# Optimization experiments

Hardware: AMD Instinct MI355X
Metric: run time of the kernel (lower is better)

The kernel has to match this reference:

```python
import jax, jax.numpy as jnp
import numpy as np

DIM = 768
B, S = 16, 1024
EPS = 1e-5


def setup_inputs() -> dict:
    key = jax.random.key(0)
    ks = jax.random.split(key, 13)
    std = 1.0 / np.sqrt(DIM)
    inp = {
        "x_A": jax.random.normal(ks[0], (B, S, DIM), jnp.float32),
        "x_B": jax.random.normal(ks[1], (B, S, DIM), jnp.float32),
        "x_C": jax.random.normal(ks[2], (B, S, DIM), jnp.float32),
        "W_q": jax.random.normal(ks[3], (DIM, DIM), jnp.float32) * std,
        "b_q": jax.random.normal(ks[4], (DIM,), jnp.float32) * std,
        "W_k": jax.random.normal(ks[5], (DIM, DIM), jnp.float32) * std,
        "b_k": jax.random.normal(ks[6], (DIM,), jnp.float32) * std,
        "W_v": jax.random.normal(ks[7], (DIM, DIM), jnp.float32) * std,
        "b_v": jax.random.normal(ks[8], (DIM,), jnp.float32) * std,
        "gamma": jnp.ones((DIM,), jnp.float32),
        "beta": jnp.zeros((DIM,), jnp.float32),
        "W_fc": jax.random.normal(ks[9], (DIM, DIM), jnp.float32) * std,
        "b_fc": jax.random.normal(ks[10], (DIM,), jnp.float32) * std,
    }
    return inp


def _linear(x, W, b):
    # torch nn.Linear: x @ W.T + b
    return jnp.einsum('bsd,ed->bse', x, W) + b


def _layernorm(x, gamma, beta):
    mu = jnp.mean(x, axis=-1, keepdims=True)
    var = jnp.mean((x - mu) ** 2, axis=-1, keepdims=True)
    return (x - mu) * jax.lax.rsqrt(var + EPS) * gamma + beta


def reference(x_A, x_B, x_C, W_q, b_q, W_k, b_k, W_v, b_v, gamma, beta, W_fc, b_fc):
    scale = 1.0 / jnp.sqrt(jnp.float32(DIM))
    Q = _linear(x_C, W_q, b_q)
    K_A = _linear(x_A, W_k, b_k)
    K_B = _linear(x_B, W_k, b_k)
    V_A = _linear(x_A, W_v, b_v)
    V_B = _linear(x_B, W_v, b_v)
    attn_A = jax.nn.softmax(jnp.einsum('bqd,bkd->bqk', Q, K_A) * scale, axis=-1)
    attn_B = jax.nn.softmax(jnp.einsum('bqd,bkd->bqk', Q, K_B) * scale, axis=-1)
    interp_A = jnp.einsum('bqk,bkd->bqd', attn_A, V_A)
    interp_B = jnp.einsum('bqk,bkd->bqd', attn_B, V_B)
    h = _layernorm(interp_A + interp_B + x_C, gamma, beta)
    return _linear(h, W_fc, b_fc)
```

## Files before the change

### kernel.cpp

```cpp
#include <hip/hip_runtime.h>

#define DIMV 768
#define BATCH 16
#define SEQ 1024
#define LN_EPS 1e-5f

typedef __attribute__((ext_vector_type(8))) short bf16x8;
typedef __attribute__((ext_vector_type(4))) float f32x4;
typedef unsigned short ushort_t;

__device__ __forceinline__ unsigned short f2bf(float f) {
    unsigned u = __float_as_uint(f);
    u = (u + 0x7FFFu + ((u >> 16) & 1u)) >> 16;
    return (unsigned short)u;
}


__global__ __launch_bounds__(512, 2) void gemm_bf16_nt_256(
    const ushort_t* __restrict__ A, const ushort_t* __restrict__ B,
    const float* __restrict__ bias, const float* __restrict__ bias2,
    void* __restrict__ Cout, void* __restrict__ Cout2,
    int K, int lda, int ldb, int ldc, float scale, int mode,
    long long sAz, long long sBz, long long sCz, int CbArg)
{
    int bx = blockIdx.x, by = blockIdx.y, bz = blockIdx.z;
    {
        const unsigned Z  = gridDim.z;
        const unsigned nx = gridDim.x, ny = gridDim.y;
        if (Z > 1) {
            const unsigned nxy = nx * ny;
            const unsigned lid = ((unsigned)bz * ny + (unsigned)by) * nx + (unsigned)bx;
            unsigned r;
            if ((Z & 7u) == 0u) {
                const unsigned c  = lid & 7u;
                const unsigned rp = lid >> 3;
                bz = (int)(c + 8u * (rp / nxy));
                r  = rp % nxy;
            } else {
                bz = (int)(lid % Z);
                r  = lid / Z;
            }
            bx = (int)(r % nx);
            by = (int)(r / nx);
        } else {
            const unsigned nwg = nx * ny;
            if ((nwg & 7u) == 0u) {
                const unsigned lid = (unsigned)by * nx + (unsigned)bx;
                const unsigned nl  = (lid & 7u) * (nwg >> 3) + (lid >> 3);
                bx = (int)(nl % nx);
                by = (int)(nl / nx);
            }
        }
    }

    A += (long long)bz * sAz;
    B += (long long)bz * sBz;
    float*    Cf  = (float*)Cout    + ((mode == 0) ? (long long)bz * sCz : 0);
    ushort_t* Ch  = (ushort_t*)Cout + ((mode == 1) ? (long long)bz * sCz : 0);
    ushort_t* Ch2 = (ushort_t*)Cout2;

    __shared__ ushort_t As[4][256 * 32];
    __shared__ ushort_t Bs[4][256 * 32];

    const int t    = threadIdx.x;
    const int wave = t >> 6;
    const int lane = t & 63;
    const int quad = lane >> 4;
    const int lr   = lane & 15;
    const int wy   = wave >> 2;
    const int wx   = wave & 3;

    const int m0 = by * 256;
    const int n0 = bx * 256;

    const ushort_t* Abase = A + (long long)m0 * lda;
    const ushort_t* Bbase = B + (long long)n0 * ldb;

    auto issue = [&](int k0, int slot) {
        #pragma unroll
        for (int i = 0; i < 2; ++i) {
            const int idx = t + 512 * i;
            const int r   = idx >> 2;
            const int q   = idx & 3;
            const int c   = (q ^ ((r >> 1) & 3)) * 8;
            __builtin_amdgcn_global_load_lds(
                (const __attribute__((address_space(1))) unsigned int*)(Abase + (long long)r * lda + k0 + c),
                (__attribute__((address_space(3))) unsigned int*)&As[slot][idx * 8], 16, 0, 0);
            __builtin_amdgcn_global_load_lds(
                (const __attribute__((address_space(1))) unsigned int*)(Bbase + (long long)r * ldb + k0 + c),
                (__attribute__((address_space(3))) unsigned int*)&Bs[slot][idx * 8], 16, 0, 0);
        }
    };

    int offA[8], offB[4];
    #pragma unroll
    for (int i = 0; i < 8; ++i) {
        const int rowA = wy * 128 + i * 16 + lr;
        offA[i] = rowA * 32 + ((quad ^ ((rowA >> 1) & 3)) * 8);
    }
    #pragma unroll
    for (int j = 0; j < 4; ++j) {
        const int rowB = wx * 64 + j * 16 + lr;
        offB[j] = rowB * 32 + ((quad ^ ((rowB >> 1) & 3)) * 8);
    }

    f32x4 acc[8][4] = {};

    const int NK = K >> 5;
    issue(0, 0);
    issue(32, 1);
    for (int ki = 0; ki < NK; ++ki) {
        const int k2 = (ki + 2 < NK) ? (ki + 2) << 5 : (NK - 1) << 5;
        issue(k2, (ki + 2) & 3);
        asm volatile("s_waitcnt vmcnt(8)" ::: "memory");
        asm volatile("s_barrier" ::: "memory");

        const ushort_t* as = &As[ki & 3][0];
        const ushort_t* bs = &Bs[ki & 3][0];
        bf16x8 af[8], bfr[4];
        #pragma unroll
        for (int i = 0; i < 8; ++i) af[i]  = *(const bf16x8*)&as[offA[i]];
        #pragma unroll
        for (int j = 0; j < 4; ++j) bfr[j] = *(const bf16x8*)&bs[offB[j]];

        __builtin_amdgcn_s_setprio(1);
        #pragma unroll
        for (int i = 0; i < 8; ++i)
            #pragma unroll
            for (int j = 0; j < 4; ++j)
                acc[i][j] = __builtin_amdgcn_mfma_f32_16x16x32_bf16(
                    af[i], bfr[j], acc[i][j], 0, 0, 0);
        __builtin_amdgcn_s_setprio(0);
    }

    #pragma unroll
    for (int j = 0; j < 4; ++j) {
        const int n = n0 + wx * 64 + j * 16 + lr;
        float bv;
        if (mode == 4) bv = (n < DIMV) ? bias[n] : bias2[n - DIMV];
        else           bv = bias ? bias[n] : 0.0f;
        #pragma unroll
        for (int i = 0; i < 8; ++i) {
            #pragma unroll
            for (int r = 0; r < 4; ++r) {
                const int m = m0 + wy * 128 + i * 16 + quad * 4 + r;
                const float val = acc[i][j][r] * scale + bv;
                if (mode == 0) {
                    Cf[(long long)m * ldc + n] = val;
                } else if (mode == 1) {
                    Ch[(long long)m * ldc + n] = f2bf(val);
                } else {
                    const int bh = m >> 10, s = m & 1023;
                    const int hf = (bh >= CbArg) ? 1 : 0;
                    const int b  = bh - (hf ? CbArg : 0);
                    if (n < DIMV) {
                        Ch[(long long)b * (2 * SEQ * DIMV) + (long long)(hf * SEQ + s) * DIMV + n] = f2bf(val);
                    } else {
                        Ch2[(long long)b * (2 * SEQ * DIMV) + (long long)(n - DIMV) * (2 * SEQ) + hf * SEQ + s] = f2bf(val);
                    }
                }
            }
        }
    }
}

__global__ __launch_bounds__(256) void gemm_bf16_nt(
    const ushort_t* __restrict__ A, const ushort_t* __restrict__ B,
    const float* __restrict__ bias, void* __restrict__ Cout,
    int K, int lda, int ldb, int ldc, float scale,
    long long sAz, long long sBz, long long sCz)
{
    int bx = blockIdx.x, by = blockIdx.y, bz = blockIdx.z;
    {
        const unsigned Z  = gridDim.z;
        const unsigned nx = gridDim.x, ny = gridDim.y;
        if (Z > 1) {
            const unsigned nxy = nx * ny;
            const unsigned lid = ((unsigned)bz * ny + (unsigned)by) * nx + (unsigned)bx;
            unsigned r;
            if ((Z & 7u) == 0u) {
                const unsigned c  = lid & 7u;
                const unsigned rp = lid >> 3;
                bz = (int)(c + 8u * (rp / nxy));
                r  = rp % nxy;
            } else {
                bz = (int)(lid % Z);
                r  = lid / Z;
            }
            bx = (int)(r % nx);
            by = (int)(r / nx);
        } else {
            const unsigned nwg = nx * ny;
            if ((nwg & 7u) == 0u) {
                const unsigned lid = (unsigned)by * nx + (unsigned)bx;
                const unsigned nl  = (lid & 7u) * (nwg >> 3) + (lid >> 3);
                bx = (int)(nl % nx);
                by = (int)(nl / nx);
            }
        }
    }

    A += (long long)bz * sAz;
    B += (long long)bz * sBz;
    float* Cf = (float*)Cout + (long long)bz * sCz;

    __shared__ ushort_t As[3][128 * 32];
    __shared__ ushort_t Bs[3][128 * 32];

    const int t    = threadIdx.x;
    const int wave = t >> 6;
    const int lane = t & 63;
    const int quad = lane >> 4;
    const int lr   = lane & 15;
    const int wy   = wave >> 1;
    const int wx   = wave & 1;

    const int m0 = by * 128;
    const int n0 = bx * 128;

    const ushort_t* Abase = A + (long long)m0 * lda;
    const ushort_t* Bbase = B + (long long)n0 * ldb;

    auto issue = [&](int k0, int slot) {
        #pragma unroll
        for (int i = 0; i < 2; ++i) {
            const int idx = t + 256 * i;
            const int r   = idx >> 2;
            const int q   = idx & 3;
            const int c   = (q ^ ((r >> 1) & 3)) * 8;
            __builtin_amdgcn_global_load_lds(
                (const __attribute__((address_space(1))) unsigned int*)(Abase + (long long)r * lda + k0 + c),
                (__attribute__((address_space(3))) unsigned int*)&As[slot][idx * 8], 16, 0, 0);
            __builtin_amdgcn_global_load_lds(
                (const __attribute__((address_space(1))) unsigned int*)(Bbase + (long long)r * ldb + k0 + c),
                (__attribute__((address_space(3))) unsigned int*)&Bs[slot][idx * 8], 16, 0, 0);
        }
    };

    int offA[4], offB[4];
    #pragma unroll
    for (int i = 0; i < 4; ++i) {
        const int rowA = wy * 64 + i * 16 + lr;
        offA[i] = rowA * 32 + ((quad ^ ((rowA >> 1) & 3)) * 8);
        const int rowB = wx * 64 + i * 16 + lr;
        offB[i] = rowB * 32 + ((quad ^ ((rowB >> 1) & 3)) * 8);
    }

    f32x4 acc[4][4] = {};

    const int NK = K >> 5;
    issue(0, 0);
    int cur = 0, nxt = 1;
    for (int ki = 0; ki < NK; ++ki) {
        const int kn = (ki + 1 < NK) ? (ki + 1) << 5 : 0;
        issue(kn, nxt);
        asm volatile("s_waitcnt vmcnt(4)" ::: "memory");
        asm volatile("s_barrier" ::: "memory");

        const ushort_t* as = &As[cur][0];
        const ushort_t* bs = &Bs[cur][0];
        bf16x8 af[4], bfr[4];
        #pragma unroll
        for (int i = 0; i < 4; ++i) af[i]  = *(const bf16x8*)&as[offA[i]];
        #pragma unroll
        for (int j = 0; j < 4; ++j) bfr[j] = *(const bf16x8*)&bs[offB[j]];

        #pragma unroll
        for (int i = 0; i < 4; ++i)
            #pragma unroll
            for (int j = 0; j < 4; ++j)
                acc[i][j] = __builtin_amdgcn_mfma_f32_16x16x32_bf16(
                    af[i], bfr[j], acc[i][j], 0, 0, 0);

        cur = nxt;
        nxt = (nxt == 2) ? 0 : nxt + 1;
    }

    #pragma unroll
    for (int j = 0; j < 4; ++j) {
        const int n = n0 + wx * 64 + j * 16 + lr;
        const float bv = bias ? bias[n] : 0.0f;
        #pragma unroll
        for (int i = 0; i < 4; ++i) {
            #pragma unroll
            for (int r = 0; r < 4; ++r) {
                const int m = m0 + wy * 64 + i * 16 + quad * 4 + r;
                Cf[(long long)m * ldc + n] = acc[i][j][r] * scale + bv;
            }
        }
    }
}

__global__ __launch_bounds__(256) void f32_to_bf16(
    const float* __restrict__ in, ushort_t* __restrict__ out)
{
    const long long i = ((long long)blockIdx.x * 256 + threadIdx.x) * 4;
    float4 v = *reinterpret_cast<const float4*>(in + i);
    ushort4 o;
    o.x = f2bf(v.x); o.y = f2bf(v.y); o.z = f2bf(v.z); o.w = f2bf(v.w);
    *reinterpret_cast<ushort4*>(out + i) = o;
}

__global__ __launch_bounds__(256) void softmax2_inplace(float* __restrict__ S)
{
    float* s = S + (long long)blockIdx.x * (2 * SEQ);
    const int t  = threadIdx.x;
    const int hf = t >> 7;
    const int tt = t & 127;
    const int base = hf * SEQ + tt * 8;
    __shared__ float red[256];

    float4 v0 = *reinterpret_cast<const float4*>(&s[base]);
    float4 v1 = *reinterpret_cast<const float4*>(&s[base + 4]);
    float mx = fmaxf(fmaxf(fmaxf(v0.x, v0.y), fmaxf(v0.z, v0.w)),
                     fmaxf(fmaxf(v1.x, v1.y), fmaxf(v1.z, v1.w)));
    red[t] = mx;
    __syncthreads();
    for (int st = 64; st > 0; st >>= 1) {
        if (tt < st) red[t] = fmaxf(red[t], red[t + st]);
        __syncthreads();
    }
    mx = red[hf << 7];
    __syncthreads();

    v0.x = __expf(v0.x - mx); v0.y = __expf(v0.y - mx);
    v0.z = __expf(v0.z - mx); v0.w = __expf(v0.w - mx);
    v1.x = __expf(v1.x - mx); v1.y = __expf(v1.y - mx);
    v1.z = __expf(v1.z - mx); v1.w = __expf(v1.w - mx);
    red[t] = (v0.x + v0.y + v0.z + v0.w) + (v1.x + v1.y + v1.z + v1.w);
    __syncthreads();
    for (int st = 64; st > 0; st >>= 1) {
        if (tt < st) red[t] += red[t + st];
        __syncthreads();
    }
    const float inv = 1.0f / red[hf << 7];

    ushort4 o0, o1;
    o0.x = f2bf(v0.x * inv); o0.y = f2bf(v0.y * inv);
    o0.z = f2bf(v0.z * inv); o0.w = f2bf(v0.w * inv);
    o1.x = f2bf(v1.x * inv); o1.y = f2bf(v1.y * inv);
    o1.z = f2bf(v1.z * inv); o1.w = f2bf(v1.w * inv);
    *reinterpret_cast<ushort4*>((ushort_t*)s + base)     = o0;
    *reinterpret_cast<ushort4*>((ushort_t*)s + base + 4) = o1;
}

__global__ __launch_bounds__(256) void add_layernorm(
    const float* __restrict__ ACC, const float* __restrict__ xC,
    const float* __restrict__ gamma, const float* __restrict__ beta,
    ushort_t* __restrict__ H)
{
    const long long row = blockIdx.x;
    const float* a = ACC + row * DIMV;
    const float* x = xC  + row * DIMV;
    ushort_t*    h = H   + row * DIMV;
    const int t = threadIdx.x;

    __shared__ float r1[256];
    __shared__ float r2[256];

    float vals[3];
    float s = 0.f, ss = 0.f;
    #pragma unroll
    for (int i = 0; i < 3; ++i) {
        const int j = t + i * 256;
        float v = a[j] + x[j];
        vals[i] = v;
        s += v; ss += v * v;
    }
    r1[t] = s; r2[t] = ss;
    __syncthreads();
    for (int st = 128; st > 0; st >>= 1) {
        if (t < st) { r1[t] += r1[t + st]; r2[t] += r2[t + st]; }
        __syncthreads();
    }
    const float mu  = r1[0] * (1.0f / DIMV);
    const float var = r2[0] * (1.0f / DIMV) - mu * mu;
    const float inv = rsqrtf(var + LN_EPS);

    #pragma unroll
    for (int i = 0; i < 3; ++i) {
        const int j = t + i * 256;
        h[j] = f2bf((vals[i] - mu) * inv * gamma[j] + beta[j]);
    }
}

extern "C" void kernel_launch(void* const* d_in, const int* in_sizes, int n_in,
                              void* d_out, int out_size, void* d_ws, size_t ws_size,
                              hipStream_t stream)
{
    const float* xA    = (const float*)d_in[0];
    const float* xB    = (const float*)d_in[1];
    const float* xC    = (const float*)d_in[2];
    const float* Wq    = (const float*)d_in[3];
    const float* bq    = (const float*)d_in[4];
    const float* Wk    = (const float*)d_in[5];
    const float* bk    = (const float*)d_in[6];
    const float* Wv    = (const float*)d_in[7];
    const float* bv    = (const float*)d_in[8];
    const float* gamma = (const float*)d_in[9];
    const float* beta  = (const float*)d_in[10];
    const float* Wfc   = (const float*)d_in[11];
    const float* bfc   = (const float*)d_in[12];
    float* out = (float*)d_out;

    const long long eW   = (long long)DIMV * DIMV;
    const long long perB = (long long)SEQ * DIMV;
    const long long perP = (long long)SEQ * SEQ;

    const long long wBytes = 4 * eW * 2;

    auto needBytes = [&](long long cb, long long sc) {
        const long long s = 8 * perP * sc;
        const long long x = 4 * perB * cb;
        return (s > x ? s : x) + 10 * perB * cb;
    };

    int CbFit = 1;
    for (int c = BATCH; c >= 1; --c) {
        const long long sc = c < 8 ? c : 8;
        if (wBytes + needBytes(c, sc) <= (long long)ws_size) { CbFit = c; break; }
    }
    const int nChunks = (BATCH + CbFit - 1) / CbFit;
    const int CbStd   = (BATCH + nChunks - 1) / nChunks;

    char* cur = (char*)d_ws;
    ushort_t* Wqb  = (ushort_t*)cur; cur += eW * 2;
    ushort_t* Wkvb = (ushort_t*)cur; cur += 2 * eW * 2;
    ushort_t* Wfcb = (ushort_t*)cur; cur += eW * 2;
    char* chunkBase = cur;

    const float scale = 0.03608439182435161f;

    f32_to_bf16<<<(int)(eW / 1024), 256, 0, stream>>>(Wq,  Wqb);
    f32_to_bf16<<<(int)(eW / 1024), 256, 0, stream>>>(Wk,  Wkvb);
    f32_to_bf16<<<(int)(eW / 1024), 256, 0, stream>>>(Wv,  Wkvb + eW);
    f32_to_bf16<<<(int)(eW / 1024), 256, 0, stream>>>(Wfc, Wfcb);

    for (int b0 = 0; b0 < BATCH; b0 += CbStd) {
        const int Cb = (b0 + CbStd <= BATCH) ? CbStd : (BATCH - b0);
        const long long off = (long long)b0 * perB;

        int SC = Cb;
        while (SC > 1 && wBytes + needBytes(Cb, SC) > (long long)ws_size) --SC;

        const long long Sbytes =
            (8 * perP * (long long)SC > 4 * perB * (long long)Cb)
                ? 8 * perP * (long long)SC : 4 * perB * (long long)Cb;

        char* p = chunkBase;
        ushort_t* xCb  = (ushort_t*)p;
        ushort_t* xABb = (ushort_t*)p;
        float*    Sf   = (float*)p;    p += Sbytes;
        ushort_t* Qb   = (ushort_t*)p; p += 2 * perB * Cb;
        ushort_t* Kb   = (ushort_t*)p;
        float*    ACC  = (float*)p;    p += 4 * perB * Cb;
        ushort_t* Vtb  = (ushort_t*)p; p += 4 * perB * Cb;

        dim3 gq  (DIMV / 256, Cb * (SEQ / 256), 1);
        dim3 gkv (2 * DIMV / 256, 2 * Cb * (SEQ / 256), 1);
        const int gcv = (int)((long long)Cb * perB / 1024);

        f32_to_bf16<<<gcv, 256, 0, stream>>>(xC + off, xCb);
        gemm_bf16_nt_256<<<gq, 512, 0, stream>>>(xCb, Wqb, bq, nullptr, Qb, nullptr,
            DIMV, DIMV, DIMV, DIMV, 1.f, 1, 0, 0, 0, 0);
        f32_to_bf16<<<gcv, 256, 0, stream>>>(xA + off, xABb);
        f32_to_bf16<<<gcv, 256, 0, stream>>>(xB + off, xABb + (long long)Cb * perB);
        gemm_bf16_nt_256<<<gkv, 512, 0, stream>>>(xABb, Wkvb, bk, bv, Kb, Vtb,
            DIMV, DIMV, DIMV, DIMV, 1.f, 4, 0, 0, 0, Cb);

        for (int s0 = 0; s0 < Cb; s0 += SC) {
            const int sc = (s0 + SC <= Cb) ? SC : (Cb - s0);
            dim3 gsc(2 * SEQ / 256, SEQ / 256, sc);
            dim3 gpv(DIMV / 128, SEQ / 128, sc);

            gemm_bf16_nt_256<<<gsc, 512, 0, stream>>>(
                Qb + (long long)s0 * perB, Kb + (long long)s0 * 2 * perB,
                nullptr, nullptr, Sf, nullptr,
                DIMV, DIMV, DIMV, 2 * SEQ, scale, 0, perB, 2 * perB, 2 * perP, 0);

            softmax2_inplace<<<sc * SEQ, 256, 0, stream>>>(Sf);

            gemm_bf16_nt<<<gpv, 256, 0, stream>>>(
                (const ushort_t*)Sf, Vtb + (long long)s0 * 2 * perB,
                nullptr, ACC + (long long)s0 * perB,
                2 * SEQ, 4 * SEQ, 2 * SEQ, DIMV, 1.f, 4 * perP, 2 * perB, perB);
        }

        add_layernorm<<<Cb * SEQ, 256, 0, stream>>>(ACC, xC + off, gamma, beta, Qb);

        gemm_bf16_nt_256<<<gq, 512, 0, stream>>>(Qb, Wfcb, bfc, nullptr, out + off, nullptr,
            DIMV, DIMV, DIMV, DIMV, 1.f, 0, 0, 0, 0, 0);
    }
}
```

Before: 636.7 us.

## Restructure GEMM main loop into four sub-phases with interleaved half-tile staging

The bf16 NT GEMM main loop now processes 64-wide K steps split into four phases. Each phase loads part of the A/B fragments from LDS, issues one half-tile global-to-LDS copy for a future K step, then runs 16 MFMAs. Shared memory is reorganised into two buffers of two K halves, replacing the 4-slot ring. The aim is finer-grained overlap of global loads, LDS reads and MFMA work, at the cost of more barriers and lgkmcnt waits per K step and tricky prefetch indexing at the tail.

```diff
diff --git a/kernel.cpp b/kernel.cpp
--- a/kernel.cpp
+++ b/kernel.cpp
@@ -59,8 +59,8 @@
     ushort_t* Ch  = (ushort_t*)Cout + ((mode == 1) ? (long long)bz * sCz : 0);
     ushort_t* Ch2 = (ushort_t*)Cout2;
 
-    __shared__ ushort_t As[4][256 * 32];
-    __shared__ ushort_t Bs[4][256 * 32];
+    __shared__ ushort_t As[2][2][256 * 32];
+    __shared__ ushort_t Bs[2][2][256 * 32];
 
     const int t    = threadIdx.x;
     const int wave = t >> 6;
@@ -76,7 +76,8 @@
     const ushort_t* Abase = A + (long long)m0 * lda;
     const ushort_t* Bbase = B + (long long)n0 * ldb;
 
-    auto issue = [&](int k0, int slot) {
+    auto stageA = [&](int jH, int kh) {
+        const int k0 = jH * 64 + kh * 32;
         #pragma unroll
         for (int i = 0; i < 2; ++i) {
             const int idx = t + 512 * i;
@@ -85,52 +86,120 @@
             const int c   = (q ^ ((r >> 1) & 3)) * 8;
             __builtin_amdgcn_global_load_lds(
                 (const __attribute__((address_space(1))) unsigned int*)(Abase + (long long)r * lda + k0 + c),
-                (__attribute__((address_space(3))) unsigned int*)&As[slot][idx * 8], 16, 0, 0);
+                (__attribute__((address_space(3))) unsigned int*)&As[jH & 1][kh][idx * 8], 16, 0, 0);
+        }
+    };
+    auto stageB = [&](int jH, int kh) {
+        const int k0 = jH * 64 + kh * 32;
+        #pragma unroll
+        for (int i = 0; i < 2; ++i) {
+            const int idx = t + 512 * i;
+            const int r   = idx >> 2;
+            const int q   = idx & 3;
+            const int c   = (q ^ ((r >> 1) & 3)) * 8;
             __builtin_amdgcn_global_load_lds(
                 (const __attribute__((address_space(1))) unsigned int*)(Bbase + (long long)r * ldb + k0 + c),
-                (__attribute__((address_space(3))) unsigned int*)&Bs[slot][idx * 8], 16, 0, 0);
+                (__attribute__((address_space(3))) unsigned int*)&Bs[jH & 1][kh][idx * 8], 16, 0, 0);
         }
     };
 
     int offA[8], offB[4];
     #pragma unroll
     for (int i = 0; i < 8; ++i) {
-        const int rowA = wy * 128 + i * 16 + lr;
-        offA[i] = rowA * 32 + ((quad ^ ((rowA >> 1) & 3)) * 8);
-    }
-    #pragma unroll
-    for (int j = 0; j < 4; ++j) {
-        const int rowB = wx * 64 + j * 16 + lr;
-        offB[j] = rowB * 32 + ((quad ^ ((rowB >> 1) & 3)) * 8);
+        const int rA = wy * 128 + i * 16 + lr;
+        offA[i] = rA * 32 + ((quad ^ ((rA >> 1) & 3)) * 8);
+    }
+    #pragma unroll
+    for (int j4 = 0; j4 < 4; ++j4) {
+        const int rB = wx * 64 + j4 * 16 + lr;
+        offB[j4] = rB * 32 + ((quad ^ ((rB >> 1) & 3)) * 8);
     }
 
     f32x4 acc[8][4] = {};
 
-    const int NK = K >> 5;
-    issue(0, 0);
-    issue(32, 1);
-    for (int ki = 0; ki < NK; ++ki) {
-        const int k2 = (ki + 2 < NK) ? (ki + 2) << 5 : (NK - 1) << 5;
-        issue(k2, (ki + 2) & 3);
-        asm volatile("s_waitcnt vmcnt(8)" ::: "memory");
-        asm volatile("s_barrier" ::: "memory");
-
-        const ushort_t* as = &As[ki & 3][0];
-        const ushort_t* bs = &Bs[ki & 3][0];
-        bf16x8 af[8], bfr[4];
-        #pragma unroll
-        for (int i = 0; i < 8; ++i) af[i]  = *(const bf16x8*)&as[offA[i]];
-        #pragma unroll
-        for (int j = 0; j < 4; ++j) bfr[j] = *(const bf16x8*)&bs[offB[j]];
-
-        __builtin_amdgcn_s_setprio(1);
-        #pragma unroll
-        for (int i = 0; i < 8; ++i)
-            #pragma unroll
-            for (int j = 0; j < 4; ++j)
-                acc[i][j] = __builtin_amdgcn_mfma_f32_16x16x32_bf16(
-                    af[i], bfr[j], acc[i][j], 0, 0, 0);
-        __builtin_amdgcn_s_setprio(0);
+    const int NK = K >> 6;
+
+    stageA(0, 0); stageB(0, 0); stageA(0, 1); stageB(0, 1);
+    stageA(1, 0); stageB(1, 0);
+    asm volatile("s_waitcnt vmcnt(4)" ::: "memory");
+    asm volatile("s_barrier" ::: "memory");
+
+    for (int j = 0; j < NK; ++j) {
+        const ushort_t* a0 = &As[j & 1][0][0];
+        const ushort_t* a1 = &As[j & 1][1][0];
+        const ushort_t* b0 = &Bs[j & 1][0][0];
+        const ushort_t* b1 = &Bs[j & 1][1][0];
+        bf16x8 bfr[4];
+
+        {
+            bf16x8 af[4];
+            #pragma unroll
+            for (int q4 = 0; q4 < 4; ++q4) bfr[q4] = *(const bf16x8*)&b0[offB[q4]];
+            #pragma unroll
+            for (int i2 = 0; i2 < 4; ++i2) af[i2] = *(const bf16x8*)&a0[offA[i2]];
+            stageA((j < NK - 1) ? j + 1 : j - 1, 1);
+            __builtin_amdgcn_s_setprio(1);
+            #pragma unroll
+            for (int i2 = 0; i2 < 4; ++i2)
+                #pragma unroll
+                for (int q4 = 0; q4 < 4; ++q4)
+                    acc[i2][q4] = __builtin_amdgcn_mfma_f32_16x16x32_bf16(
+                        af[i2], bfr[q4], acc[i2][q4], 0, 0, 0);
+            __builtin_amdgcn_s_setprio(0);
+            asm volatile("s_waitcnt lgkmcnt(0)" ::: "memory");
+            asm volatile("s_barrier" ::: "memory");
+        }
+        {
+            bf16x8 af[4];
+            #pragma unroll
+            for (int i2 = 0; i2 < 4; ++i2) af[i2] = *(const bf16x8*)&a0[offA[4 + i2]];
+            stageB((j < NK - 1) ? j + 1 : j - 1, 1);
+            __builtin_amdgcn_s_setprio(1);
+            #pragma unroll
+            for (int i2 = 0; i2 < 4; ++i2)
+                #pragma unroll
+                for (int q4 = 0; q4 < 4; ++q4)
+                    acc[4 + i2][q4] = __builtin_amdgcn_mfma_f32_16x16x32_bf16(
+                        af[i2], bfr[q4], acc[4 + i2][q4], 0, 0, 0);
+            __builtin_amdgcn_s_setprio(0);
+            asm volatile("s_waitcnt lgkmcnt(0)" ::: "memory");
+            asm volatile("s_barrier" ::: "memory");
+        }
+        {
+            bf16x8 af[4];
+            #pragma unroll
+            for (int q4 = 0; q4 < 4; ++q4) bfr[q4] = *(const bf16x8*)&b1[offB[q4]];
+            #pragma unroll
+            for (int i2 = 0; i2 < 4; ++i2) af[i2] = *(const bf16x8*)&a1[offA[i2]];
+            stageA((j < NK - 2) ? j + 2 : j, 0);
+            __builtin_amdgcn_s_setprio(1);
+            #pragma unroll
+            for (int i2 = 0; i2 < 4; ++i2)
+                #pragma unroll
+                for (int q4 = 0; q4 < 4; ++q4)
+                    acc[i2][q4] = __builtin_amdgcn_mfma_f32_16x16x32_bf16(
+                        af[i2], bfr[q4], acc[i2][q4], 0, 0, 0);
+            __builtin_amdgcn_s_setprio(0);
+            asm volatile("s_waitcnt lgkmcnt(0)" ::: "memory");
+            asm volatile("s_barrier" ::: "memory");
+        }
+        {
+            bf16x8 af[4];
+            #pragma unroll
+            for (int i2 = 0; i2 < 4; ++i2) af[i2] = *(const bf16x8*)&a1[offA[4 + i2]];
+            stageB((j < NK - 2) ? j + 2 : j, 0);
+            __builtin_amdgcn_s_setprio(1);
+            #pragma unroll
+            for (int i2 = 0; i2 < 4; ++i2)
+                #pragma unroll
+                for (int q4 = 0; q4 < 4; ++q4)
+                    acc[4 + i2][q4] = __builtin_amdgcn_mfma_f32_16x16x32_bf16(
+                        af[i2], bfr[q4], acc[4 + i2][q4], 0, 0, 0);
+            __builtin_amdgcn_s_setprio(0);
+            asm volatile("s_waitcnt lgkmcnt(0)" ::: "memory");
+            asm volatile("s_waitcnt vmcnt(4)" ::: "memory");
+            asm volatile("s_barrier" ::: "memory");
+        }
     }
 
     #pragma unroll
```

Measured after the change: 638.8 us. Within noise of the previous version (+0.3%).
